# Performance work log

Measured on AMD Instinct MI355X. Metric: run time of the kernel, lower is better.

The kernel has to match this reference:

```python
import jax, jax.numpy as jnp
import numpy as np
import math

EMBED_DIM = 768
NUM_HEADS = 12
HEAD_DIM = EMBED_DIM // NUM_HEADS
B, L = 8, 1024


def setup_inputs() -> dict:
    key = jax.random.key(0)
    ks = jax.random.split(key, 10)
    s = 1.0 / math.sqrt(EMBED_DIM)
    x = jax.random.normal(ks[0], (B, L, EMBED_DIM), dtype=jnp.float32)
    attention_mask = jnp.ones((B, L), dtype=jnp.int32)
    # torch nn.Linear weights: shape (out, in), y = x @ W.T + b
    Wq = jax.random.normal(ks[1], (EMBED_DIM, EMBED_DIM), jnp.float32) * s
    bq = jnp.zeros((EMBED_DIM,), jnp.float32)
    Wk = jax.random.normal(ks[2], (EMBED_DIM, EMBED_DIM), jnp.float32) * s
    bk = jnp.zeros((EMBED_DIM,), jnp.float32)
    Wv = jax.random.normal(ks[3], (EMBED_DIM, EMBED_DIM), jnp.float32) * s
    bv = jnp.zeros((EMBED_DIM,), jnp.float32)
    Wo = jax.random.normal(ks[4], (EMBED_DIM, EMBED_DIM), jnp.float32) * s
    bo = jnp.zeros((EMBED_DIM,), jnp.float32)
    return {"x": x, "attention_mask": attention_mask,
            "Wq": Wq, "bq": bq, "Wk": Wk, "bk": bk,
            "Wv": Wv, "bv": bv, "Wo": Wo, "bo": bo}


def reference(x, attention_mask, Wq, bq, Wk, bk, Wv, bv, Wo, bo):
    # NOTE: faithful to the original buggy forward:
    #   V = K_embed(x); scores = K @ K^T; Q unused; scale by sqrt(embed_dim);
    #   mask broadcasts over the KEY axis (masks entire query rows).
    b, l, d = x.shape
    K = x @ Wk.T + bk                                  # (B,L,D)
    Q = x @ Wq.T + bq                                  # computed but unused (as in source)
    V = K                                              # V = self.K_embed(x)
    Kh = K.reshape(b, l, NUM_HEADS, HEAD_DIM).transpose(0, 2, 1, 3)  # (B,H,L,dh)
    Vh = V.reshape(b, l, NUM_HEADS, HEAD_DIM).transpose(0, 2, 1, 3)
    scores = jnp.einsum('bhid,bhjd->bhij', Kh, Kh) / math.sqrt(EMBED_DIM)
    if attention_mask is not None:
        row_mask = attention_mask[:, None, :, None]    # (B,1,L,1) -> masks query rows
        scores = jnp.where(row_mask == 0, jnp.float32(-1e9), scores)
    attn = jax.nn.softmax(scores, axis=-1)             # dropout p=0 -> identity
    wV = jnp.einsum('bhij,bhjd->bhid', attn, Vh)       # (B,H,L,dh)
    wV = wV.transpose(0, 2, 1, 3).reshape(b, l, d)     # (B,L,D)
    out = wV @ Wo.T + bo
    return out
```

## Files before the change

kernel.cpp:

```cpp
#include <hip/hip_runtime.h>
#include <hip/hip_bf16.h>

#define NUM_B 8
#define SEQ 1024
#define DIM 768
#define NH 12
#define DH 64

typedef __attribute__((ext_vector_type(8))) short bf16x8;
typedef __attribute__((ext_vector_type(4))) float floatx4;
typedef __attribute__((ext_vector_type(4))) unsigned short ushortx4;
typedef __attribute__((ext_vector_type(8))) unsigned short ushortx8;

__device__ __forceinline__ unsigned short f2bf(float f) {
  unsigned u = __float_as_uint(f);
  u += 0x7FFFu + ((u >> 16) & 1u);
  return (unsigned short)(u >> 16);
}

#define GLOAD16(g, l) __builtin_amdgcn_global_load_lds( \
    (const __attribute__((address_space(1))) unsigned int*)(g), \
    (__attribute__((address_space(3))) unsigned int*)(l), 16, 0, 0)

__global__ __launch_bounds__(256) void convert_kernel(
    const float* __restrict__ x, const float* __restrict__ Wk,
    const float* __restrict__ Wo, unsigned short* __restrict__ xb,
    unsigned short* __restrict__ Wkb, unsigned short* __restrict__ Wob)
{
  const int NX4 = (8192 * 768) / 4;
  const int NW4 = (768 * 768) / 4;
  int i = blockIdx.x * 256 + threadIdx.x;
  const float* s; unsigned short* d; int off;
  if (i < NX4)            { s = x;  d = xb;  off = i; }
  else if (i < NX4 + NW4) { s = Wk; d = Wkb; off = i - NX4; }
  else                    { s = Wo; d = Wob; off = i - NX4 - NW4; }
  float4 v = ((const float4*)s)[off];
  ushortx4 h;
  h.x = f2bf(v.x); h.y = f2bf(v.y); h.z = f2bf(v.z); h.w = f2bf(v.w);
  ((ushortx4*)d)[off] = h;
}

__global__ __launch_bounds__(256) void proj_k_kernel(
    const unsigned short* __restrict__ xb, const unsigned short* __restrict__ Wkb,
    const float* __restrict__ bk, unsigned short* __restrict__ Kbh,
    unsigned short* __restrict__ KbhT)
{
  __shared__ __align__(16) unsigned short smem[24576];
  const int tid = threadIdx.x;
  const int lane = tid & 63;
  const int w = tid >> 6;
  const int wr = w >> 1, wc = w & 1;
  const int quad = lane >> 4, r16 = lane & 15;
  const int m0 = blockIdx.x * 64, n0 = blockIdx.y * 128;
  const int wbase = (tid & ~63);

  floatx4 acc[2][4] = {};

  auto stage = [&](int kt, int buf) {
    unsigned short* As = smem + buf * 12288;
    unsigned short* Bs = As + 4096;
#pragma unroll
    for (int i = 0; i < 2; ++i) {
      int c = tid + i * 256;
      int row = c >> 3, ch = c & 7;
      GLOAD16(xb + (size_t)(m0 + row) * DIM + kt + ch * 8,
              As + (size_t)(wbase + i * 256) * 8);
    }
#pragma unroll
    for (int i = 0; i < 4; ++i) {
      int c = tid + i * 256;
      int row = c >> 3, ch = c & 7;
      GLOAD16(Wkb + (size_t)(n0 + row) * DIM + kt + ch * 8,
              Bs + (size_t)(wbase + i * 256) * 8);
    }
  };

  stage(0, 0);
  int buf = 0;
  for (int it = 0; it < 12; ++it) {
    __syncthreads();
    if (it + 1 < 12) stage((it + 1) * 64, buf ^ 1);
    const unsigned short* As = smem + buf * 12288;
    const unsigned short* Bs = As + 4096;
    bf16x8 af[2][2], bfm[4][2];
#pragma unroll
    for (int mi = 0; mi < 2; ++mi)
#pragma unroll
      for (int kc = 0; kc < 2; ++kc)
        af[mi][kc] = *(const bf16x8*)&As[(wr * 32 + mi * 16 + r16) * 64 + kc * 32 + quad * 8];
#pragma unroll
    for (int ni = 0; ni < 4; ++ni)
#pragma unroll
      for (int kc = 0; kc < 2; ++kc)
        bfm[ni][kc] = *(const bf16x8*)&Bs[(wc * 64 + ni * 16 + r16) * 64 + kc * 32 + quad * 8];
#pragma unroll
    for (int mi = 0; mi < 2; ++mi)
#pragma unroll
      for (int ni = 0; ni < 4; ++ni) {
        acc[mi][ni] = __builtin_amdgcn_mfma_f32_16x16x32_bf16(af[mi][0], bfm[ni][0], acc[mi][ni], 0, 0, 0);
        acc[mi][ni] = __builtin_amdgcn_mfma_f32_16x16x32_bf16(af[mi][1], bfm[ni][1], acc[mi][ni], 0, 0, 0);
      }
    buf ^= 1;
  }

  __syncthreads();
  unsigned short* Ct = smem;
  const int bb = m0 >> 10, l0 = m0 & 1023;
#pragma unroll
  for (int mi = 0; mi < 2; ++mi)
#pragma unroll
    for (int ni = 0; ni < 4; ++ni) {
      int col = n0 + wc * 64 + ni * 16 + r16;
      float bias = bk[col];
      int hh = col >> 6, dd = col & 63;
      ushortx4 pk;
#pragma unroll
      for (int r = 0; r < 4; ++r) {
        int mrow = wr * 32 + mi * 16 + quad * 4 + r;
        unsigned short us = f2bf(acc[mi][ni][r] + bias);
        Kbh[((size_t)(bb * NH + hh) * SEQ + l0 + mrow) * DH + dd] = us;
        pk[r] = us;
      }
      *(ushortx4*)&Ct[(wc * 64 + ni * 16 + r16) * 72 + wr * 32 + mi * 16 + quad * 4] = pk;
    }
  __syncthreads();
#pragma unroll
  for (int i = 0; i < 4; ++i) {
    int c = tid + i * 256;
    int row = c >> 3, ch = c & 7;
    ushortx8 v = *(const ushortx8*)&Ct[row * 72 + ch * 8];
    int j = n0 + row;
    int hh = j >> 6, dd = j & 63;
    *(ushortx8*)&KbhT[((size_t)(bb * NH + hh) * DH + dd) * SEQ + l0 + ch * 8] = v;
  }
}

__global__ __launch_bounds__(256) void attn_kernel(
    const unsigned short* __restrict__ Kbh, const unsigned short* __restrict__ KbhT,
    const int* __restrict__ mask, unsigned short* __restrict__ wV)
{
  __shared__ __align__(16) unsigned short smem[25600];
  unsigned short* Ps = smem + 16384;

  const int tid = threadIdx.x;
  const int lane = tid & 63;
  const int w = tid >> 6;
  const int quad = lane >> 4, r16 = lane & 15;
  const int qt = blockIdx.x, bh = blockIdx.y;
  const int b = bh / NH, h = bh % NH;
  const unsigned short* Kb  = Kbh  + (size_t)bh * SEQ * DH;
  const unsigned short* KbT = KbhT + (size_t)bh * DH * SEQ;
  const int q0 = qt * 128;
  const int wbase = (tid & ~63);
  const float SCALE = 0.036084391824351615f;

  bf16x8 aq[2][2];
#pragma unroll
  for (int mi = 0; mi < 2; ++mi)
#pragma unroll
    for (int kc = 0; kc < 2; ++kc)
      aq[mi][kc] = *(const bf16x8*)(Kb + (size_t)(q0 + w * 32 + mi * 16 + r16) * DH + kc * 32 + quad * 8);

  bool mok[2][4];
#pragma unroll
  for (int mi = 0; mi < 2; ++mi)
#pragma unroll
    for (int r = 0; r < 4; ++r)
      mok[mi][r] = (mask[b * SEQ + q0 + w * 32 + mi * 16 + quad * 4 + r] != 0);

  floatx4 accO[2][4] = {};
  float psum[2][4] = {};

  auto stage = [&](int kt, int buf) {
    unsigned short* Ks  = smem + buf * 4096;
    unsigned short* KTs = smem + 8192 + buf * 4096;
#pragma unroll
    for (int i = 0; i < 2; ++i) {
      int c = tid + i * 256;
      GLOAD16(Kb + (size_t)kt * DH + (size_t)c * 8,
              Ks + (size_t)(wbase + i * 256) * 8);
    }
#pragma unroll
    for (int i = 0; i < 2; ++i) {
      int c = tid + i * 256;
      int row = c >> 3, ch = c & 7;
      GLOAD16(KbT + (size_t)row * SEQ + kt + ch * 8,
              KTs + (size_t)(wbase + i * 256) * 8);
    }
  };

  stage(0, 0);
  int buf = 0;
  for (int it = 0; it < SEQ / 64; ++it) {
    __syncthreads();
    if (it + 1 < SEQ / 64) stage((it + 1) * 64, buf ^ 1);
    const unsigned short* Ks  = smem + buf * 4096;
    const unsigned short* KTs = smem + 8192 + buf * 4096;

    floatx4 S[2][4] = {};
#pragma unroll
    for (int ni = 0; ni < 4; ++ni) {
      bf16x8 b0 = *(const bf16x8*)&Ks[(ni * 16 + r16) * 64 + quad * 8];
      bf16x8 b1 = *(const bf16x8*)&Ks[(ni * 16 + r16) * 64 + 32 + quad * 8];
#pragma unroll
      for (int mi = 0; mi < 2; ++mi) {
        S[mi][ni] = __builtin_amdgcn_mfma_f32_16x16x32_bf16(aq[mi][0], b0, S[mi][ni], 0, 0, 0);
        S[mi][ni] = __builtin_amdgcn_mfma_f32_16x16x32_bf16(aq[mi][1], b1, S[mi][ni], 0, 0, 0);
      }
    }

#pragma unroll
    for (int mi = 0; mi < 2; ++mi)
#pragma unroll
      for (int r = 0; r < 4; ++r) {
        int prow = (w * 32 + mi * 16 + quad * 4 + r) * 72;
#pragma unroll
        for (int ni = 0; ni < 4; ++ni) {
          float p = mok[mi][r] ? __expf(S[mi][ni][r] * SCALE) : 1.0f;
          psum[mi][r] += p;
          Ps[prow + ni * 16 + r16] = f2bf(p);
        }
      }

    bf16x8 ap[2][2];
#pragma unroll
    for (int mi = 0; mi < 2; ++mi)
#pragma unroll
      for (int kc = 0; kc < 2; ++kc)
        ap[mi][kc] = *(const bf16x8*)&Ps[(w * 32 + mi * 16 + r16) * 72 + kc * 32 + quad * 8];
#pragma unroll
    for (int ni = 0; ni < 4; ++ni) {
      bf16x8 v0 = *(const bf16x8*)&KTs[(ni * 16 + r16) * 64 + quad * 8];
      bf16x8 v1 = *(const bf16x8*)&KTs[(ni * 16 + r16) * 64 + 32 + quad * 8];
#pragma unroll
      for (int mi = 0; mi < 2; ++mi) {
        accO[mi][ni] = __builtin_amdgcn_mfma_f32_16x16x32_bf16(ap[mi][0], v0, accO[mi][ni], 0, 0, 0);
        accO[mi][ni] = __builtin_amdgcn_mfma_f32_16x16x32_bf16(ap[mi][1], v1, accO[mi][ni], 0, 0, 0);
      }
    }
    buf ^= 1;
  }

  float rinv[2][4];
#pragma unroll
  for (int mi = 0; mi < 2; ++mi)
#pragma unroll
    for (int r = 0; r < 4; ++r) {
      float s = psum[mi][r];
      s += __shfl_xor(s, 1);
      s += __shfl_xor(s, 2);
      s += __shfl_xor(s, 4);
      s += __shfl_xor(s, 8);
      rinv[mi][r] = 1.0f / s;
    }
#pragma unroll
  for (int mi = 0; mi < 2; ++mi)
#pragma unroll
    for (int ni = 0; ni < 4; ++ni)
#pragma unroll
      for (int r = 0; r < 4; ++r) {
        int l = q0 + w * 32 + mi * 16 + quad * 4 + r;
        int col = h * DH + ni * 16 + r16;
        wV[(size_t)(b * SEQ + l) * DIM + col] = f2bf(accO[mi][ni][r] * rinv[mi][r]);
      }
}

__global__ __launch_bounds__(256) void proj_o_kernel(
    const unsigned short* __restrict__ wVb, const unsigned short* __restrict__ Wob,
    const float* __restrict__ bo, float* __restrict__ out)
{
  __shared__ __align__(16) unsigned short smem[24576];
  const int tid = threadIdx.x;
  const int lane = tid & 63;
  const int w = tid >> 6;
  const int wr = w >> 1, wc = w & 1;
  const int quad = lane >> 4, r16 = lane & 15;
  const int m0 = blockIdx.x * 64, n0 = blockIdx.y * 128;
  const int wbase = (tid & ~63);

  floatx4 acc[2][4] = {};

  auto stage = [&](int kt, int buf) {
    unsigned short* As = smem + buf * 12288;
    unsigned short* Bs = As + 4096;
#pragma unroll
    for (int i = 0; i < 2; ++i) {
      int c = tid + i * 256;
      int row = c >> 3, ch = c & 7;
      GLOAD16(wVb + (size_t)(m0 + row) * DIM + kt + ch * 8,
              As + (size_t)(wbase + i * 256) * 8);
    }
#pragma unroll
    for (int i = 0; i < 4; ++i) {
      int c = tid + i * 256;
      int row = c >> 3, ch = c & 7;
      GLOAD16(Wob + (size_t)(n0 + row) * DIM + kt + ch * 8,
              Bs + (size_t)(wbase + i * 256) * 8);
    }
  };

  stage(0, 0);
  int buf = 0;
  for (int it = 0; it < 12; ++it) {
    __syncthreads();
    if (it + 1 < 12) stage((it + 1) * 64, buf ^ 1);
    const unsigned short* As = smem + buf * 12288;
    const unsigned short* Bs = As + 4096;
    bf16x8 af[2][2], bfm[4][2];
#pragma unroll
    for (int mi = 0; mi < 2; ++mi)
#pragma unroll
      for (int kc = 0; kc < 2; ++kc)
        af[mi][kc] = *(const bf16x8*)&As[(wr * 32 + mi * 16 + r16) * 64 + kc * 32 + quad * 8];
#pragma unroll
    for (int ni = 0; ni < 4; ++ni)
#pragma unroll
      for (int kc = 0; kc < 2; ++kc)
        bfm[ni][kc] = *(const bf16x8*)&Bs[(wc * 64 + ni * 16 + r16) * 64 + kc * 32 + quad * 8];
#pragma unroll
    for (int mi = 0; mi < 2; ++mi)
#pragma unroll
      for (int ni = 0; ni < 4; ++ni) {
        acc[mi][ni] = __builtin_amdgcn_mfma_f32_16x16x32_bf16(af[mi][0], bfm[ni][0], acc[mi][ni], 0, 0, 0);
        acc[mi][ni] = __builtin_amdgcn_mfma_f32_16x16x32_bf16(af[mi][1], bfm[ni][1], acc[mi][ni], 0, 0, 0);
      }
    buf ^= 1;
  }

#pragma unroll
  for (int mi = 0; mi < 2; ++mi)
#pragma unroll
    for (int ni = 0; ni < 4; ++ni) {
      int col = n0 + wc * 64 + ni * 16 + r16;
      float bias = bo[col];
#pragma unroll
      for (int r = 0; r < 4; ++r) {
        int row = m0 + wr * 32 + mi * 16 + quad * 4 + r;
        out[(size_t)row * DIM + col] = acc[mi][ni][r] + bias;
      }
    }
}

extern "C" void kernel_launch(void* const* d_in, const int* in_sizes, int n_in,
                              void* d_out, int out_size, void* d_ws, size_t ws_size,
                              hipStream_t stream) {
  const float* x  = (const float*)d_in[0];
  const int* mask = (const int*)d_in[1];
  const float* Wk = (const float*)d_in[4];
  const float* bk = (const float*)d_in[5];
  const float* Wo = (const float*)d_in[8];
  const float* bo = (const float*)d_in[9];
  float* out = (float*)d_out;

  unsigned short* p = (unsigned short*)d_ws;
  unsigned short* xb   = p;  p += (size_t)8192 * 768;
  unsigned short* Wkb  = p;  p += (size_t)768 * 768;
  unsigned short* Wob  = p;  p += (size_t)768 * 768;
  unsigned short* Kbh  = p;  p += (size_t)NUM_B * NH * SEQ * DH;
  unsigned short* KbhT = p;  p += (size_t)NUM_B * NH * SEQ * DH;
  unsigned short* wVb  = p;

  convert_kernel<<<7296, 256, 0, stream>>>(x, Wk, Wo, xb, Wkb, Wob);
  proj_k_kernel<<<dim3(128, 6), 256, 0, stream>>>(xb, Wkb, bk, Kbh, KbhT);
  attn_kernel<<<dim3(8, NUM_B * NH), 256, 0, stream>>>(Kbh, KbhT, mask, wVb);
  proj_o_kernel<<<dim3(128, 6), 256, 0, stream>>>(wVb, Wob, bo, out);
}
```

Baseline: 185.5 us.

## XOR-swizzle LDS tiles, enlarge GEMM tiles, split out K transpose kernel

Applies XOR swizzling to LDS staging in the projection and attention kernels to reduce bank conflicts. The GEMMs move to 128x128 tiles with single buffering instead of 64x128 double buffering. The K transpose moves out of the projection epilogue into its own kernel. Attention swaps the grid order so heads are the fast axis, uses exp2f with a prescaled constant, and shrinks the P row stride to 68. The trade-offs are an extra kernel launch, an extra round trip for the K tensor, and no overlap between global loads and MFMA in the GEMMs.

```diff
diff --git a/kernel.cpp b/kernel.cpp
--- a/kernel.cpp
+++ b/kernel.cpp
@@ -42,96 +42,105 @@
 
 __global__ __launch_bounds__(256) void proj_k_kernel(
     const unsigned short* __restrict__ xb, const unsigned short* __restrict__ Wkb,
-    const float* __restrict__ bk, unsigned short* __restrict__ Kbh,
-    unsigned short* __restrict__ KbhT)
-{
-  __shared__ __align__(16) unsigned short smem[24576];
+    const float* __restrict__ bk, unsigned short* __restrict__ Kbh)
+{
+  __shared__ __align__(16) unsigned short smem[16384];
+  unsigned short* As = smem;
+  unsigned short* Bs = smem + 8192;
+
   const int tid = threadIdx.x;
   const int lane = tid & 63;
   const int w = tid >> 6;
   const int wr = w >> 1, wc = w & 1;
   const int quad = lane >> 4, r16 = lane & 15;
-  const int m0 = blockIdx.x * 64, n0 = blockIdx.y * 128;
+  const int rs = r16 & 7;
+  const int m0 = blockIdx.x * 128, n0 = blockIdx.y * 128;
   const int wbase = (tid & ~63);
 
-  floatx4 acc[2][4] = {};
-
-  auto stage = [&](int kt, int buf) {
-    unsigned short* As = smem + buf * 12288;
-    unsigned short* Bs = As + 4096;
-#pragma unroll
-    for (int i = 0; i < 2; ++i) {
-      int c = tid + i * 256;
-      int row = c >> 3, ch = c & 7;
-      GLOAD16(xb + (size_t)(m0 + row) * DIM + kt + ch * 8,
+  floatx4 acc[4][4] = {};
+
+  for (int kt = 0; kt < DIM; kt += 64) {
+    __syncthreads();
+#pragma unroll
+    for (int i = 0; i < 4; ++i) {
+      int c = tid + i * 256;
+      int row = c >> 3, g = (c & 7) ^ (row & 7);
+      GLOAD16(xb + (size_t)(m0 + row) * DIM + kt + g * 8,
               As + (size_t)(wbase + i * 256) * 8);
     }
 #pragma unroll
     for (int i = 0; i < 4; ++i) {
       int c = tid + i * 256;
-      int row = c >> 3, ch = c & 7;
-      GLOAD16(Wkb + (size_t)(n0 + row) * DIM + kt + ch * 8,
+      int row = c >> 3, g = (c & 7) ^ (row & 7);
+      GLOAD16(Wkb + (size_t)(n0 + row) * DIM + kt + g * 8,
               Bs + (size_t)(wbase + i * 256) * 8);
     }
-  };
-
-  stage(0, 0);
-  int buf = 0;
-  for (int it = 0; it < 12; ++it) {
-    __syncthreads();
-    if (it + 1 < 12) stage((it + 1) * 64, buf ^ 1);
-    const unsigned short* As = smem + buf * 12288;
-    const unsigned short* Bs = As + 4096;
-    bf16x8 af[2][2], bfm[4][2];
-#pragma unroll
-    for (int mi = 0; mi < 2; ++mi)
-#pragma unroll
-      for (int kc = 0; kc < 2; ++kc)
-        af[mi][kc] = *(const bf16x8*)&As[(wr * 32 + mi * 16 + r16) * 64 + kc * 32 + quad * 8];
+    __syncthreads();
+
+    bf16x8 af[4][2], bfm[4][2];
+#pragma unroll
+    for (int mi = 0; mi < 4; ++mi)
+#pragma unroll
+      for (int kc = 0; kc < 2; ++kc)
+        af[mi][kc] = *(const bf16x8*)&As[(wr * 64 + mi * 16 + r16) * 64 + ((kc * 4 + quad) ^ rs) * 8];
 #pragma unroll
     for (int ni = 0; ni < 4; ++ni)
 #pragma unroll
       for (int kc = 0; kc < 2; ++kc)
-        bfm[ni][kc] = *(const bf16x8*)&Bs[(wc * 64 + ni * 16 + r16) * 64 + kc * 32 + quad * 8];
-#pragma unroll
-    for (int mi = 0; mi < 2; ++mi)
+        bfm[ni][kc] = *(const bf16x8*)&Bs[(wc * 64 + ni * 16 + r16) * 64 + ((kc * 4 + quad) ^ rs) * 8];
+#pragma unroll
+    for (int mi = 0; mi < 4; ++mi)
 #pragma unroll
       for (int ni = 0; ni < 4; ++ni) {
         acc[mi][ni] = __builtin_amdgcn_mfma_f32_16x16x32_bf16(af[mi][0], bfm[ni][0], acc[mi][ni], 0, 0, 0);
         acc[mi][ni] = __builtin_amdgcn_mfma_f32_16x16x32_bf16(af[mi][1], bfm[ni][1], acc[mi][ni], 0, 0, 0);
       }
-    buf ^= 1;
-  }
-
-  __syncthreads();
-  unsigned short* Ct = smem;
-  const int bb = m0 >> 10, l0 = m0 & 1023;
-#pragma unroll
-  for (int mi = 0; mi < 2; ++mi)
+  }
+
+#pragma unroll
+  for (int mi = 0; mi < 4; ++mi)
 #pragma unroll
     for (int ni = 0; ni < 4; ++ni) {
       int col = n0 + wc * 64 + ni * 16 + r16;
       float bias = bk[col];
       int hh = col >> 6, dd = col & 63;
-      ushortx4 pk;
 #pragma unroll
       for (int r = 0; r < 4; ++r) {
-        int mrow = wr * 32 + mi * 16 + quad * 4 + r;
-        unsigned short us = f2bf(acc[mi][ni][r] + bias);
-        Kbh[((size_t)(bb * NH + hh) * SEQ + l0 + mrow) * DH + dd] = us;
-        pk[r] = us;
-      }
-      *(ushortx4*)&Ct[(wc * 64 + ni * 16 + r16) * 72 + wr * 32 + mi * 16 + quad * 4] = pk;
-    }
+        int row = m0 + wr * 64 + mi * 16 + quad * 4 + r;
+        int bb = row >> 10, ll = row & 1023;
+        Kbh[((size_t)(bb * NH + hh) * SEQ + ll) * DH + dd] = f2bf(acc[mi][ni][r] + bias);
+      }
+    }
+}
+
+__global__ __launch_bounds__(256) void transpose_kernel(
+    const unsigned short* __restrict__ Kbh, unsigned short* __restrict__ KbhT)
+{
+  __shared__ __align__(16) unsigned short Ts[4096];
+  const int tid = threadIdx.x;
+  const int bh = blockIdx.x, lt = blockIdx.y;
+  const int l0 = lt * 64;
+  const unsigned short* src = Kbh + (size_t)bh * SEQ * DH;
+  unsigned short* dst = KbhT + (size_t)bh * DH * SEQ;
+  const int wbase = (tid & ~63);
+
+#pragma unroll
+  for (int i = 0; i < 2; ++i) {
+    int c = tid + i * 256;
+    int row = c >> 3, g = (c & 7) ^ (row & 7);
+    GLOAD16(src + (size_t)(l0 + row) * DH + g * 8,
+            Ts + (size_t)(wbase + i * 256) * 8);
+  }
   __syncthreads();
 #pragma unroll
-  for (int i = 0; i < 4; ++i) {
+  for (int i = 0; i < 2; ++i) {
     int c = tid + i * 256;
-    int row = c >> 3, ch = c & 7;
-    ushortx8 v = *(const ushortx8*)&Ct[row * 72 + ch * 8];
-    int j = n0 + row;
-    int hh = j >> 6, dd = j & 63;
-    *(ushortx8*)&KbhT[((size_t)(bb * NH + hh) * DH + dd) * SEQ + l0 + ch * 8] = v;
+    int d = c >> 3, ch = c & 7;
+    ushortx8 v;
+#pragma unroll
+    for (int j = 0; j < 8; ++j)
+      v[j] = Ts[(ch * 8 + j) * 64 + (((d >> 3) ^ j) * 8) + (d & 7)];
+    *(ushortx8*)&dst[(size_t)d * SEQ + l0 + ch * 8] = v;
   }
 }
 
@@ -139,20 +148,21 @@
     const unsigned short* __restrict__ Kbh, const unsigned short* __restrict__ KbhT,
     const int* __restrict__ mask, unsigned short* __restrict__ wV)
 {
-  __shared__ __align__(16) unsigned short smem[25600];
+  __shared__ __align__(16) unsigned short smem[25088];
   unsigned short* Ps = smem + 16384;
 
   const int tid = threadIdx.x;
   const int lane = tid & 63;
   const int w = tid >> 6;
   const int quad = lane >> 4, r16 = lane & 15;
-  const int qt = blockIdx.x, bh = blockIdx.y;
+  const int rs = r16 & 7;
+  const int bh = blockIdx.x, qt = blockIdx.y;
   const int b = bh / NH, h = bh % NH;
   const unsigned short* Kb  = Kbh  + (size_t)bh * SEQ * DH;
   const unsigned short* KbT = KbhT + (size_t)bh * DH * SEQ;
   const int q0 = qt * 128;
   const int wbase = (tid & ~63);
-  const float SCALE = 0.036084391824351615f;
+  const float SC2 = 0.05205809663084291f;
 
   bf16x8 aq[2][2];
 #pragma unroll
@@ -177,14 +187,15 @@
 #pragma unroll
     for (int i = 0; i < 2; ++i) {
       int c = tid + i * 256;
-      GLOAD16(Kb + (size_t)kt * DH + (size_t)c * 8,
+      int row = c >> 3, g = (c & 7) ^ (row & 7);
+      GLOAD16(Kb + (size_t)(kt + row) * DH + g * 8,
               Ks + (size_t)(wbase + i * 256) * 8);
     }
 #pragma unroll
     for (int i = 0; i < 2; ++i) {
       int c = tid + i * 256;
-      int row = c >> 3, ch = c & 7;
-      GLOAD16(KbT + (size_t)row * SEQ + kt + ch * 8,
+      int row = c >> 3, g = (c & 7) ^ (row & 7);
+      GLOAD16(KbT + (size_t)row * SEQ + kt + g * 8,
               KTs + (size_t)(wbase + i * 256) * 8);
     }
   };
@@ -200,8 +211,9 @@
     floatx4 S[2][4] = {};
 #pragma unroll
     for (int ni = 0; ni < 4; ++ni) {
-      bf16x8 b0 = *(const bf16x8*)&Ks[(ni * 16 + r16) * 64 + quad * 8];
-      bf16x8 b1 = *(const bf16x8*)&Ks[(ni * 16 + r16) * 64 + 32 + quad * 8];
+      int rb = (ni * 16 + r16) * 64;
+      bf16x8 b0 = *(const bf16x8*)&Ks[rb + ((quad) ^ rs) * 8];
+      bf16x8 b1 = *(const bf16x8*)&Ks[rb + ((4 + quad) ^ rs) * 8];
 #pragma unroll
       for (int mi = 0; mi < 2; ++mi) {
         S[mi][ni] = __builtin_amdgcn_mfma_f32_16x16x32_bf16(aq[mi][0], b0, S[mi][ni], 0, 0, 0);
@@ -213,10 +225,10 @@
     for (int mi = 0; mi < 2; ++mi)
 #pragma unroll
       for (int r = 0; r < 4; ++r) {
-        int prow = (w * 32 + mi * 16 + quad * 4 + r) * 72;
+        int prow = (w * 32 + mi * 16 + quad * 4 + r) * 68;
 #pragma unroll
         for (int ni = 0; ni < 4; ++ni) {
-          float p = mok[mi][r] ? __expf(S[mi][ni][r] * SCALE) : 1.0f;
+          float p = mok[mi][r] ? exp2f(S[mi][ni][r] * SC2) : 1.0f;
           psum[mi][r] += p;
           Ps[prow + ni * 16 + r16] = f2bf(p);
         }
@@ -227,11 +239,12 @@
     for (int mi = 0; mi < 2; ++mi)
 #pragma unroll
       for (int kc = 0; kc < 2; ++kc)
-        ap[mi][kc] = *(const bf16x8*)&Ps[(w * 32 + mi * 16 + r16) * 72 + kc * 32 + quad * 8];
+        ap[mi][kc] = *(const bf16x8*)&Ps[(w * 32 + mi * 16 + r16) * 68 + kc * 32 + quad * 8];
 #pragma unroll
     for (int ni = 0; ni < 4; ++ni) {
-      bf16x8 v0 = *(const bf16x8*)&KTs[(ni * 16 + r16) * 64 + quad * 8];
-      bf16x8 v1 = *(const bf16x8*)&KTs[(ni * 16 + r16) * 64 + 32 + quad * 8];
+      int rb = (ni * 16 + r16) * 64;
+      bf16x8 v0 = *(const bf16x8*)&KTs[rb + ((quad) ^ rs) * 8];
+      bf16x8 v1 = *(const bf16x8*)&KTs[rb + ((4 + quad) ^ rs) * 8];
 #pragma unroll
       for (int mi = 0; mi < 2; ++mi) {
         accO[mi][ni] = __builtin_amdgcn_mfma_f32_16x16x32_bf16(ap[mi][0], v0, accO[mi][ni], 0, 0, 0);
@@ -269,73 +282,68 @@
     const unsigned short* __restrict__ wVb, const unsigned short* __restrict__ Wob,
     const float* __restrict__ bo, float* __restrict__ out)
 {
-  __shared__ __align__(16) unsigned short smem[24576];
+  __shared__ __align__(16) unsigned short smem[16384];
+  unsigned short* As = smem;
+  unsigned short* Bs = smem + 8192;
+
   const int tid = threadIdx.x;
   const int lane = tid & 63;
   const int w = tid >> 6;
   const int wr = w >> 1, wc = w & 1;
   const int quad = lane >> 4, r16 = lane & 15;
-  const int m0 = blockIdx.x * 64, n0 = blockIdx.y * 128;
+  const int rs = r16 & 7;
+  const int m0 = blockIdx.x * 128, n0 = blockIdx.y * 128;
   const int wbase = (tid & ~63);
 
-  floatx4 acc[2][4] = {};
-
-  auto stage = [&](int kt, int buf) {
-    unsigned short* As = smem + buf * 12288;
-    unsigned short* Bs = As + 4096;
-#pragma unroll
-    for (int i = 0; i < 2; ++i) {
-      int c = tid + i * 256;
-      int row = c >> 3, ch = c & 7;
-      GLOAD16(wVb + (size_t)(m0 + row) * DIM + kt + ch * 8,
+  floatx4 acc[4][4] = {};
+
+  for (int kt = 0; kt < DIM; kt += 64) {
+    __syncthreads();
+#pragma unroll
+    for (int i = 0; i < 4; ++i) {
+      int c = tid + i * 256;
+      int row = c >> 3, g = (c & 7) ^ (row & 7);
+      GLOAD16(wVb + (size_t)(m0 + row) * DIM + kt + g * 8,
               As + (size_t)(wbase + i * 256) * 8);
     }
 #pragma unroll
     for (int i = 0; i < 4; ++i) {
       int c = tid + i * 256;
-      int row = c >> 3, ch = c & 7;
-      GLOAD16(Wob + (size_t)(n0 + row) * DIM + kt + ch * 8,
+      int row = c >> 3, g = (c & 7) ^ (row & 7);
+      GLOAD16(Wob + (size_t)(n0 + row) * DIM + kt + g * 8,
               Bs + (size_t)(wbase + i * 256) * 8);
     }
-  };
-
-  stage(0, 0);
-  int buf = 0;
-  for (int it = 0; it < 12; ++it) {
-    __syncthreads();
-    if (it + 1 < 12) stage((it + 1) * 64, buf ^ 1);
-    const unsigned short* As = smem + buf * 12288;
-    const unsigned short* Bs = As + 4096;
-    bf16x8 af[2][2], bfm[4][2];
-#pragma unroll
-    for (int mi = 0; mi < 2; ++mi)
-#pragma unroll
-      for (int kc = 0; kc < 2; ++kc)
-        af[mi][kc] = *(const bf16x8*)&As[(wr * 32 + mi * 16 + r16) * 64 + kc * 32 + quad * 8];
+    __syncthreads();
+
+    bf16x8 af[4][2], bfm[4][2];
+#pragma unroll
+    for (int mi = 0; mi < 4; ++mi)
+#pragma unroll
+      for (int kc = 0; kc < 2; ++kc)
+        af[mi][kc] = *(const bf16x8*)&As[(wr * 64 + mi * 16 + r16) * 64 + ((kc * 4 + quad) ^ rs) * 8];
 #pragma unroll
     for (int ni = 0; ni < 4; ++ni)
 #pragma unroll
       for (int kc = 0; kc < 2; ++kc)
-        bfm[ni][kc] = *(const bf16x8*)&Bs[(wc * 64 + ni * 16 + r16) * 64 + kc * 32 + quad * 8];
-#pragma unroll
-    for (int mi = 0; mi < 2; ++mi)
+        bfm[ni][kc] = *(const bf16x8*)&Bs[(wc * 64 + ni * 16 + r16) * 64 + ((kc * 4 + quad) ^ rs) * 8];
+#pragma unroll
+    for (int mi = 0; mi < 4; ++mi)
 #pragma unroll
       for (int ni = 0; ni < 4; ++ni) {
         acc[mi][ni] = __builtin_amdgcn_mfma_f32_16x16x32_bf16(af[mi][0], bfm[ni][0], acc[mi][ni], 0, 0, 0);
         acc[mi][ni] = __builtin_amdgcn_mfma_f32_16x16x32_bf16(af[mi][1], bfm[ni][1], acc[mi][ni], 0, 0, 0);
       }
-    buf ^= 1;
-  }
-
-#pragma unroll
-  for (int mi = 0; mi < 2; ++mi)
+  }
+
+#pragma unroll
+  for (int mi = 0; mi < 4; ++mi)
 #pragma unroll
     for (int ni = 0; ni < 4; ++ni) {
       int col = n0 + wc * 64 + ni * 16 + r16;
       float bias = bo[col];
 #pragma unroll
       for (int r = 0; r < 4; ++r) {
-        int row = m0 + wr * 32 + mi * 16 + quad * 4 + r;
+        int row = m0 + wr * 64 + mi * 16 + quad * 4 + r;
         out[(size_t)row * DIM + col] = acc[mi][ni][r] + bias;
       }
     }
@@ -361,7 +369,8 @@
   unsigned short* wVb  = p;
 
   convert_kernel<<<7296, 256, 0, stream>>>(x, Wk, Wo, xb, Wkb, Wob);
-  proj_k_kernel<<<dim3(128, 6), 256, 0, stream>>>(xb, Wkb, bk, Kbh, KbhT);
-  attn_kernel<<<dim3(8, NUM_B * NH), 256, 0, stream>>>(Kbh, KbhT, mask, wVb);
-  proj_o_kernel<<<dim3(128, 6), 256, 0, stream>>>(wVb, Wob, bo, out);
-}
+  proj_k_kernel<<<dim3(64, 6), 256, 0, stream>>>(xb, Wkb, bk, Kbh);
+  transpose_kernel<<<dim3(NUM_B * NH, 16), 256, 0, stream>>>(Kbh, KbhT);
+  attn_kernel<<<dim3(NUM_B * NH, 8), 256, 0, stream>>>(Kbh, KbhT, mask, wVb);
+  proj_o_kernel<<<dim3(64, 6), 256, 0, stream>>>(wVb, Wob, bo, out);
+}
```

New measurement: 208.4 us. +12.4%, slower.
